# Performance work log

Hardware: AMD Instinct MI355X
Metric: run time of the kernel (lower is better)

The kernel has to match this reference:

```python
import jax, jax.numpy as jnp
import numpy as np

DIM = 4096
N_HEADS_Q = 32
N_HEADS_KV = 8
N_REP = N_HEADS_Q // N_HEADS_KV
HEAD_DIM = DIM // N_HEADS_Q


def setup_inputs() -> dict:
    key = jax.random.key(0)
    k0, k1, k2, k3, k4 = jax.random.split(key, 5)
    B, S = 2, 2048
    scale = 1.0 / np.sqrt(DIM)
    return {
        "x": jax.random.normal(k0, (B, S, DIM), dtype=jnp.float32),
        "wq": jax.random.normal(k1, (DIM, N_HEADS_Q * HEAD_DIM), dtype=jnp.float32) * scale,
        "wk": jax.random.normal(k2, (DIM, N_HEADS_KV * HEAD_DIM), dtype=jnp.float32) * scale,
        "wv": jax.random.normal(k3, (DIM, N_HEADS_KV * HEAD_DIM), dtype=jnp.float32) * scale,
        "wo": jax.random.normal(k4, (DIM, DIM), dtype=jnp.float32) * scale,
        "start_pos": 0,
    }


def reference(x, wq, wk, wv, wo, start_pos):
    # use_cache=False path: fresh causal self-attention with GQA.
    B, S, _ = x.shape
    q = (x @ wq).reshape(B, S, N_HEADS_Q, HEAD_DIM)
    k = (x @ wk).reshape(B, S, N_HEADS_KV, HEAD_DIM)
    v = (x @ wv).reshape(B, S, N_HEADS_KV, HEAD_DIM)
    # repeat_kv: each kv head repeated N_REP times contiguously along head axis
    k = jnp.repeat(k, N_REP, axis=2)  # [B, S, Hq, D]
    v = jnp.repeat(v, N_REP, axis=2)
    att = jnp.einsum("bqhd,bkhd->bhqk", q, k) / np.sqrt(HEAD_DIM).astype(np.float32)
    causal = jnp.tril(jnp.ones((S, S), dtype=bool))  # [S, S]
    att = jnp.where(causal[None, None, :, :], att, -jnp.inf)
    scores = jax.nn.softmax(att, axis=-1)
    out = jnp.einsum("bhqk,bkhd->bqhd", scores, v).reshape(B, S, DIM)
    return out @ wo
```

## Files before the change

### kernel.cpp

```cpp
#include <hip/hip_runtime.h>
#include <cstdint>


typedef __bf16 bf16;
typedef __bf16 bf16x4 __attribute__((ext_vector_type(4)));
typedef __bf16 bf16x8 __attribute__((ext_vector_type(8)));
typedef float f32x4 __attribute__((ext_vector_type(4)));
typedef float f32x16 __attribute__((ext_vector_type(16)));

#define DEV_INLINE __device__ __forceinline__

DEV_INLINE void load_lds16(const bf16* g, bf16* l) {
  __builtin_amdgcn_global_load_lds(
      (const __attribute__((address_space(1))) void*)g,
      (__attribute__((address_space(3))) void*)l, 16, 0, 0);
}

DEV_INLINE unsigned pk2(float a, float b) {
  union { bf16 v[2]; unsigned u; } t;
  t.v[0] = (bf16)a; t.v[1] = (bf16)b;
  return t.u;
}

__global__ __launch_bounds__(256) void cast_f32_bf16(const float* __restrict__ in,
                                                     bf16* __restrict__ out, int n) {
  int i = (blockIdx.x * 256 + threadIdx.x) * 8;
  if (i >= n) return;
  float4 a = *(const float4*)(in + i);
  float4 b = *(const float4*)(in + i + 4);
  bf16x8 o;
  o[0] = (bf16)a.x; o[1] = (bf16)a.y; o[2] = (bf16)a.z; o[3] = (bf16)a.w;
  o[4] = (bf16)b.x; o[5] = (bf16)b.y; o[6] = (bf16)b.z; o[7] = (bf16)b.w;
  *(bf16x8*)(out + i) = o;
}

__global__ __launch_bounds__(256) void transpose_cast_all(
    const float* __restrict__ wq, const float* __restrict__ wk,
    const float* __restrict__ wv, const float* __restrict__ wo,
    bf16* __restrict__ wt, bf16* __restrict__ wot, float qscale) {
  __shared__ float t[32][33];
  int bx = blockIdx.x, k0 = blockIdx.y * 32;
  const float* src;
  bf16* dst;
  int N, ncol0, nrow0;
  float scale = 1.0f;
  if (bx < 128) {
    src = wq; dst = wt; N = 4096; ncol0 = bx * 32; nrow0 = ncol0; scale = qscale;
  } else if (bx < 160) {
    src = wk; dst = wt; N = 1024; ncol0 = (bx - 128) * 32; nrow0 = 4096 + ncol0;
  } else if (bx < 192) {
    src = wv; dst = wt; N = 1024; ncol0 = (bx - 160) * 32; nrow0 = 5120 + ncol0;
  } else {
    src = wo; dst = wot; N = 4096; ncol0 = (bx - 192) * 32; nrow0 = ncol0;
  }
  int tx = threadIdx.x, ty = threadIdx.y;
#pragma unroll
  for (int i = 0; i < 32; i += 8)
    t[ty + i][tx] = src[(size_t)(k0 + ty + i) * N + ncol0 + tx];
  __syncthreads();
#pragma unroll
  for (int i = 0; i < 32; i += 8)
    dst[(size_t)(nrow0 + ty + i) * 4096 + k0 + tx] = (bf16)(t[tx][ty + i] * scale);
}

__global__ __launch_bounds__(256) void transpose_v(const bf16* __restrict__ qkv,
                                                   bf16* __restrict__ vt) {
  __shared__ bf16 t[32][33];
  int s0 = blockIdx.x * 32, d0 = blockIdx.y * 32, bh = blockIdx.z;
  int b = bh >> 3, h = bh & 7;
  int tx = threadIdx.x, ty = threadIdx.y;
#pragma unroll
  for (int i = 0; i < 32; i += 8)
    t[ty + i][tx] =
        qkv[(size_t)(b * 2048 + s0 + ty + i) * 6144 + 5120 + h * 128 + d0 + tx];
  __syncthreads();
#pragma unroll
  for (int i = 0; i < 32; i += 8)
    vt[((size_t)bh * 128 + d0 + ty + i) * 2048 + s0 + tx] = t[tx][ty + i];
}

template <typename OT>
__global__ __launch_bounds__(512, 2) void gemm_bt8(const bf16* __restrict__ A,
                                                   const bf16* __restrict__ Bt,
                                                   OT* __restrict__ C,
                                                   int M, int N, int K) {
  __shared__ __align__(16) bf16 lds[2][4][128 * 64];
  const int t = threadIdx.x, w = t >> 6, l = t & 63;
  const int lr = l & 15, lh = l >> 4;
  const int rm = w >> 2, cn = w & 3;
  const int mBase = blockIdx.y * 256, nBase = blockIdx.x * 256;
  const int NT = K >> 6;

  size_t gA0[2], gB0[2];
#pragma unroll
  for (int it = 0; it < 2; it++) {
    int c = it * 512 + t;
    int idx = c >> 3;
    int kc = (c & 7) ^ (idx & 7);
    gA0[it] = (size_t)(mBase + (idx >> 6) * 128 + (idx & 63)) * K + kc * 8;
    gB0[it] = (size_t)(nBase + (idx >> 5) * 64 + (idx & 31)) * K + kc * 8;
  }
  const size_t strideA1 = (size_t)64 * K;
  const size_t strideB1 = (size_t)32 * K;
  const int ldst0 = (w * 64) * 8, ldst1 = (512 + w * 64) * 8;

#define STAGE_Q(tile, q, base, off0, off1)                                  \
  do {                                                                      \
    int th_ = (tile);                                                       \
    if (th_ < NT) {                                                         \
      bf16* qb_ = &lds[th_ & 1][q][0];                                      \
      size_t ka_ = (size_t)th_ * 64;                                        \
      load_lds16((base) + (off0) + ka_, qb_ + ldst0);                       \
      load_lds16((base) + (off1) + ka_, qb_ + ldst1);                       \
    }                                                                       \
  } while (0)
#define STAGE_A0(tile) STAGE_Q(tile, 0, A, gA0[0], gA0[1])
#define STAGE_B0(tile) STAGE_Q(tile, 1, Bt, gB0[0], gB0[1])
#define STAGE_B1(tile) STAGE_Q(tile, 2, Bt, gB0[0] + strideB1, gB0[1] + strideB1)
#define STAGE_A1(tile) STAGE_Q(tile, 3, A, gA0[0] + strideA1, gA0[1] + strideA1)

  STAGE_A0(0); STAGE_B0(0); STAGE_B1(0); STAGE_A1(0);
  STAGE_A0(1); STAGE_B0(1); STAGE_B1(1);

  f32x4 acc[8][4] = {};
  bf16x8 aF[4][2], bLo[2][2], bHi[2][2];
  const int rowA = (rm * 64 + lr) * 64;
  const int colB = (cn * 32 + lr) * 64;
  const int xo0 = ((lh ^ (lr & 7)) << 3);
  const int xo1 = (((4 + lh) ^ (lr & 7)) << 3);

  for (int T = 0; T < NT; T++) {
    if (T < NT - 1) asm volatile("s_waitcnt vmcnt(6)" ::: "memory");
    else            asm volatile("s_waitcnt vmcnt(0)" ::: "memory");
    __builtin_amdgcn_s_barrier();
    const bf16* q0 = &lds[T & 1][0][0];
    const bf16* q1 = &lds[T & 1][1][0];
    const bf16* q2 = &lds[T & 1][2][0];
    const bf16* q3 = &lds[T & 1][3][0];

#pragma unroll
    for (int mi = 0; mi < 4; mi++) {
      aF[mi][0] = *(const bf16x8*)(q0 + rowA + mi * 1024 + xo0);
      aF[mi][1] = *(const bf16x8*)(q0 + rowA + mi * 1024 + xo1);
    }
#pragma unroll
    for (int ni = 0; ni < 2; ni++) {
      bLo[ni][0] = *(const bf16x8*)(q1 + colB + ni * 1024 + xo0);
      bLo[ni][1] = *(const bf16x8*)(q1 + colB + ni * 1024 + xo1);
    }
    STAGE_A1(T + 1);

    __builtin_amdgcn_s_setprio(1);
#pragma unroll
    for (int ks = 0; ks < 2; ks++)
#pragma unroll
      for (int mi = 0; mi < 4; mi++)
#pragma unroll
        for (int ni = 0; ni < 2; ni++)
          acc[mi][ni] = __builtin_amdgcn_mfma_f32_16x16x32_bf16(
              aF[mi][ks], bLo[ni][ks], acc[mi][ni], 0, 0, 0);
    __builtin_amdgcn_s_setprio(0);
#pragma unroll
    for (int ni = 0; ni < 2; ni++) {
      bHi[ni][0] = *(const bf16x8*)(q2 + colB + ni * 1024 + xo0);
      bHi[ni][1] = *(const bf16x8*)(q2 + colB + ni * 1024 + xo1);
    }

    __builtin_amdgcn_sched_barrier(0);
    __builtin_amdgcn_s_barrier();
    __builtin_amdgcn_sched_barrier(0);
    STAGE_A0(T + 2);

    __builtin_amdgcn_s_setprio(1);
#pragma unroll
    for (int ks = 0; ks < 2; ks++)
#pragma unroll
      for (int mi = 0; mi < 4; mi++)
#pragma unroll
        for (int ni = 0; ni < 2; ni++)
          acc[mi][2 + ni] = __builtin_amdgcn_mfma_f32_16x16x32_bf16(
              aF[mi][ks], bHi[ni][ks], acc[mi][2 + ni], 0, 0, 0);
    __builtin_amdgcn_s_setprio(0);
#pragma unroll
    for (int mi = 0; mi < 4; mi++) {
      aF[mi][0] = *(const bf16x8*)(q3 + rowA + mi * 1024 + xo0);
      aF[mi][1] = *(const bf16x8*)(q3 + rowA + mi * 1024 + xo1);
    }
    STAGE_B0(T + 2);

    __builtin_amdgcn_s_setprio(1);
#pragma unroll
    for (int ks = 0; ks < 2; ks++)
#pragma unroll
      for (int mi = 0; mi < 4; mi++)
#pragma unroll
        for (int ni = 0; ni < 2; ni++)
          acc[4 + mi][ni] = __builtin_amdgcn_mfma_f32_16x16x32_bf16(
              aF[mi][ks], bLo[ni][ks], acc[4 + mi][ni], 0, 0, 0);
    __builtin_amdgcn_s_setprio(0);
    STAGE_B1(T + 2);

    __builtin_amdgcn_s_setprio(1);
#pragma unroll
    for (int ks = 0; ks < 2; ks++)
#pragma unroll
      for (int mi = 0; mi < 4; mi++)
#pragma unroll
        for (int ni = 0; ni < 2; ni++)
          acc[4 + mi][2 + ni] = __builtin_amdgcn_mfma_f32_16x16x32_bf16(
              aF[mi][ks], bHi[ni][ks], acc[4 + mi][2 + ni], 0, 0, 0);
    __builtin_amdgcn_s_setprio(0);
  }
#undef STAGE_Q
#undef STAGE_A0
#undef STAGE_B0
#undef STAGE_B1
#undef STAGE_A1

#pragma unroll
  for (int mi = 0; mi < 8; mi++)
#pragma unroll
    for (int ni = 0; ni < 4; ni++) {
      int row = mBase + rm * 128 + mi * 16 + lh * 4;
      int col = nBase + cn * 64 + ni * 16 + lr;
#pragma unroll
      for (int r = 0; r < 4; r++)
        C[(size_t)(row + r) * N + col] = (OT)acc[mi][ni][r];
    }
}

__global__ __launch_bounds__(256, 2) void flash_attn(const bf16* __restrict__ qkv,
                                                     const bf16* __restrict__ vt,
                                                     bf16* __restrict__ ao) {
  __shared__ __align__(16) bf16 Ks[2][64 * 128];
  __shared__ __align__(16) bf16 Vts[2][128 * 64];
  const int t = threadIdx.x, w = t >> 6, l = t & 63;
  const int l31 = l & 31, hi = l >> 5;
  const int h = blockIdx.y, b = blockIdx.z;
  const int hkv = h >> 2;

#define STAGE_KV(kt_, buf_)                                                   \
  do {                                                                        \
    const int kb_ = (kt_) * 64;                                               \
    _Pragma("unroll")                                                         \
    for (int p = 0; p < 4; p++) {                                             \
      int c = p * 256 + t;                                                    \
      int ldsoff = (p * 256 + w * 64) * 8;                                    \
      int krow = c >> 4, kj = (c & 15) ^ (krow & 15);                         \
      load_lds16(qkv + (size_t)(b * 2048 + kb_ + krow) * 6144 + 4096 +        \
                     hkv * 128 + kj * 8,                                      \
                 &Ks[buf_][ldsoff]);                                          \
      int vrow = c >> 3, vj = (c & 7) ^ (vrow & 7);                           \
      load_lds16(vt + ((size_t)(b * 8 + hkv) * 128 + vrow) * 2048 + kb_ +     \
                     vj * 8,                                                  \
                 &Vts[buf_][ldsoff]);                                         \
    }                                                                         \
  } while (0)

  for (int phase = 0; phase < 2; phase++) {
    const int qt = phase == 0 ? blockIdx.x : 15 - blockIdx.x;
    const int qrow0 = qt * 128 + w * 32;
    const int nkt = 2 * qt + 2;
    const int q = qrow0 + l31;

    STAGE_KV(0, 0);

    bf16x8 qf[8];
#pragma unroll
    for (int d0 = 0; d0 < 8; d0++)
      qf[d0] = *(const bf16x8*)&qkv[(size_t)(b * 2048 + q) * 6144 + h * 128 +
                                    d0 * 16 + hi * 8];

    f32x16 oacc[4] = {};
    float mrow = -3.0e38f, lsum = 0.f;

    asm volatile("s_waitcnt vmcnt(0)" ::: "memory");
    __builtin_amdgcn_s_barrier();

    for (int kt = 0; kt < nkt; kt++) {
      const int cur = kt & 1;
      const int kbase = kt * 64;
      if (kt + 1 < nkt) STAGE_KV(kt + 1, cur ^ 1);

      f32x16 s[2] = {};
      __builtin_amdgcn_s_setprio(1);
#pragma unroll
      for (int d0 = 0; d0 < 8; d0++)
#pragma unroll
        for (int ct = 0; ct < 2; ct++) {
          int krow = ct * 32 + l31;
          bf16x8 kf = *(const bf16x8*)&Ks[cur][(krow * 16 +
                                                ((d0 * 2 + hi) ^ (krow & 15))) * 8];
          s[ct] = __builtin_amdgcn_mfma_f32_32x32x16_bf16(kf, qf[d0], s[ct], 0, 0, 0);
        }
      __builtin_amdgcn_s_setprio(0);

      if (kt >= 2 * qt) {
#pragma unroll
        for (int ct = 0; ct < 2; ct++)
#pragma unroll
          for (int reg = 0; reg < 16; reg++) {
            int ki = kbase + ct * 32 + (reg & 3) + 8 * (reg >> 2) + 4 * hi;
            if (ki > q) s[ct][reg] = -3.0e38f;
          }
      }

      float tm[16];
#pragma unroll
      for (int i = 0; i < 16; i++) tm[i] = fmaxf(s[0][i], s[1][i]);
#pragma unroll
      for (int st = 8; st > 0; st >>= 1)
#pragma unroll
        for (int i = 0; i < 8; i++)
          if (i < st) tm[i] = fmaxf(tm[i], tm[i + st]);
      float mx = fmaxf(tm[0], __shfl_xor(tm[0], 32));
      float mnew = fmaxf(mrow, mx);
      float al = exp2f(mrow - mnew);
      mrow = mnew;
#pragma unroll
      for (int ct = 0; ct < 2; ct++)
#pragma unroll
        for (int reg = 0; reg < 16; reg++) s[ct][reg] = exp2f(s[ct][reg] - mnew);
      float ts[16];
#pragma unroll
      for (int i = 0; i < 16; i++) ts[i] = s[0][i] + s[1][i];
#pragma unroll
      for (int st = 8; st > 0; st >>= 1)
#pragma unroll
        for (int i = 0; i < 8; i++)
          if (i < st) ts[i] = ts[i] + ts[i + st];
      float rs = ts[0] + __shfl_xor(ts[0], 32);
      lsum = lsum * al + rs;

#pragma unroll
      for (int db = 0; db < 4; db++)
#pragma unroll
        for (int reg = 0; reg < 16; reg++) oacc[db][reg] *= al;

      bf16x8 pb[4];
#pragma unroll
      for (int ks = 0; ks < 4; ks++) {
        const int ct = ks >> 1, s1 = ks & 1;
        unsigned A0 = pk2(s[ct][(2 * s1) * 4 + 0], s[ct][(2 * s1) * 4 + 1]);
        unsigned A1 = pk2(s[ct][(2 * s1) * 4 + 2], s[ct][(2 * s1) * 4 + 3]);
        unsigned B0 = pk2(s[ct][(2 * s1 + 1) * 4 + 0], s[ct][(2 * s1 + 1) * 4 + 1]);
        unsigned B1 = pk2(s[ct][(2 * s1 + 1) * 4 + 2], s[ct][(2 * s1 + 1) * 4 + 3]);
        unsigned z0 = hi ? A0 : B0, z1 = hi ? A1 : B1;
        unsigned x0 = __shfl_xor(z0, 32), x1 = __shfl_xor(z1, 32);
        union { unsigned u[4]; bf16x8 v; } pw;
        pw.u[0] = hi ? x0 : A0;
        pw.u[1] = hi ? x1 : A1;
        pw.u[2] = hi ? B0 : x0;
        pw.u[3] = hi ? B1 : x1;
        pb[ks] = pw.v;
      }

      __builtin_amdgcn_s_setprio(1);
#pragma unroll
      for (int ks = 0; ks < 4; ks++)
#pragma unroll
        for (int db = 0; db < 4; db++) {
          int vr = db * 32 + l31;
          bf16x8 vf = *(const bf16x8*)&Vts[cur][(vr * 8 +
                                                 ((ks * 2 + hi) ^ (vr & 7))) * 8];
          oacc[db] = __builtin_amdgcn_mfma_f32_32x32x16_bf16(vf, pb[ks], oacc[db], 0, 0, 0);
        }
      __builtin_amdgcn_s_setprio(0);

      asm volatile("s_waitcnt vmcnt(0)" ::: "memory");
      __builtin_amdgcn_s_barrier();
    }

    float inv = 1.0f / lsum;
#pragma unroll
    for (int db = 0; db < 4; db++)
#pragma unroll
      for (int q4 = 0; q4 < 4; q4++) {
        bf16x4 o4;
#pragma unroll
        for (int j = 0; j < 4; j++) o4[j] = (bf16)(oacc[db][q4 * 4 + j] * inv);
        int d0 = db * 32 + q4 * 8 + hi * 4;
        *(bf16x4*)&ao[(size_t)(b * 2048 + q) * 4096 + h * 128 + d0] = o4;
      }
  }
#undef STAGE_KV
}

extern "C" void kernel_launch(void* const* d_in, const int* in_sizes, int n_in,
                              void* d_out, int out_size, void* d_ws, size_t ws_size,
                              hipStream_t stream) {
  const float* x = (const float*)d_in[0];
  const float* wq = (const float*)d_in[1];
  const float* wk = (const float*)d_in[2];
  const float* wv = (const float*)d_in[3];
  const float* wo = (const float*)d_in[4];
  float* out = (float*)d_out;

  char* ws = (char*)d_ws;
  bf16* xb = (bf16*)(ws + 0);
  bf16* wt = (bf16*)(ws + 33554432);
  bf16* wot = (bf16*)(ws + 83886080);
  bf16* qkv = (bf16*)(ws + 117440512);
  bf16* vt = (bf16*)(ws + 167772160);
  bf16* ao = (bf16*)(ws + 176160768);
  if (ws_size < 209715200u) return;

  const float qscale = 0.08838834764831845f * 1.4426950408889634f;

  cast_f32_bf16<<<8192, 256, 0, stream>>>(x, xb, 16777216);
  transpose_cast_all<<<dim3(320, 128), dim3(32, 8), 0, stream>>>(
      wq, wk, wv, wo, wt, wot, qscale);

  gemm_bt8<bf16><<<dim3(24, 16), 512, 0, stream>>>(xb, wt, qkv, 4096, 6144, 4096);
  transpose_v<<<dim3(64, 4, 16), dim3(32, 8), 0, stream>>>(qkv, vt);
  flash_attn<<<dim3(8, 32, 2), 256, 0, stream>>>(qkv, vt, ao);
  gemm_bt8<float><<<dim3(16, 16), 512, 0, stream>>>(ao, wot, out, 4096, 4096, 4096);
}
```

Measured before the change: 667.7 us.

## Retile QKV GEMM to 256x192 blocks and widen weight transpose tiles

The GEMM is templated on the number of 64-column B units, with LDS reorganised into 64x64 units. The QKV projection now uses 256x192 tiles, giving 512 blocks instead of 384 so the work balances better across the CUs. The weight transpose-cast kernel moves to 64x64 tiles with float4 loads and bf16x4 stores to cut memory transactions. The narrower tile lowers arithmetic intensity per block, and the vmcnt wait counts are hand-tuned to each variant, which risks subtle pipeline mistakes.

```diff
diff --git a/kernel.cpp b/kernel.cpp
--- a/kernel.cpp
+++ b/kernel.cpp
@@ -38,29 +38,39 @@
     const float* __restrict__ wq, const float* __restrict__ wk,
     const float* __restrict__ wv, const float* __restrict__ wo,
     bf16* __restrict__ wt, bf16* __restrict__ wot, float qscale) {
-  __shared__ float t[32][33];
-  int bx = blockIdx.x, k0 = blockIdx.y * 32;
+  __shared__ float sm[64][65];
+  const int bx = blockIdx.x, k0 = blockIdx.y * 64;
   const float* src;
   bf16* dst;
   int N, ncol0, nrow0;
   float scale = 1.0f;
-  if (bx < 128) {
-    src = wq; dst = wt; N = 4096; ncol0 = bx * 32; nrow0 = ncol0; scale = qscale;
-  } else if (bx < 160) {
-    src = wk; dst = wt; N = 1024; ncol0 = (bx - 128) * 32; nrow0 = 4096 + ncol0;
-  } else if (bx < 192) {
-    src = wv; dst = wt; N = 1024; ncol0 = (bx - 160) * 32; nrow0 = 5120 + ncol0;
+  if (bx < 64) {
+    src = wq; dst = wt; N = 4096; ncol0 = bx * 64; nrow0 = ncol0; scale = qscale;
+  } else if (bx < 80) {
+    src = wk; dst = wt; N = 1024; ncol0 = (bx - 64) * 64; nrow0 = 4096 + ncol0;
+  } else if (bx < 96) {
+    src = wv; dst = wt; N = 1024; ncol0 = (bx - 80) * 64; nrow0 = 5120 + ncol0;
   } else {
-    src = wo; dst = wot; N = 4096; ncol0 = (bx - 192) * 32; nrow0 = ncol0;
-  }
-  int tx = threadIdx.x, ty = threadIdx.y;
-#pragma unroll
-  for (int i = 0; i < 32; i += 8)
-    t[ty + i][tx] = src[(size_t)(k0 + ty + i) * N + ncol0 + tx];
+    src = wo; dst = wot; N = 4096; ncol0 = (bx - 96) * 64; nrow0 = ncol0;
+  }
+  const int t = threadIdx.x;
+  const int r16 = t >> 4, c4 = (t & 15) * 4;
+#pragma unroll
+  for (int i = 0; i < 4; i++) {
+    int row = r16 + i * 16;
+    float4 v = *(const float4*)&src[(size_t)(k0 + row) * N + ncol0 + c4];
+    sm[row][c4 + 0] = v.x; sm[row][c4 + 1] = v.y;
+    sm[row][c4 + 2] = v.z; sm[row][c4 + 3] = v.w;
+  }
   __syncthreads();
 #pragma unroll
-  for (int i = 0; i < 32; i += 8)
-    dst[(size_t)(nrow0 + ty + i) * 4096 + k0 + tx] = (bf16)(t[tx][ty + i] * scale);
+  for (int i = 0; i < 4; i++) {
+    int nr = r16 + i * 16;
+    bf16x4 o;
+#pragma unroll
+    for (int j = 0; j < 4; j++) o[j] = (bf16)(sm[c4 + j][nr] * scale);
+    *(bf16x4*)&dst[(size_t)(nrow0 + nr) * 4096 + k0 + c4] = o;
+  }
 }
 
 __global__ __launch_bounds__(256) void transpose_v(const bf16* __restrict__ qkv,
@@ -79,76 +89,80 @@
     vt[((size_t)bh * 128 + d0 + ty + i) * 2048 + s0 + tx] = t[tx][ty + i];
 }
 
-template <typename OT>
+template <typename OT, int NBU>
 __global__ __launch_bounds__(512, 2) void gemm_bt8(const bf16* __restrict__ A,
                                                    const bf16* __restrict__ Bt,
                                                    OT* __restrict__ C,
                                                    int M, int N, int K) {
-  __shared__ __align__(16) bf16 lds[2][4][128 * 64];
+  constexpr int NU = 4 + NBU;
+  __shared__ __align__(16) bf16 lds[2][NU][64 * 64];
   const int t = threadIdx.x, w = t >> 6, l = t & 63;
   const int lr = l & 15, lh = l >> 4;
   const int rm = w >> 2, cn = w & 3;
-  const int mBase = blockIdx.y * 256, nBase = blockIdx.x * 256;
+  const int mBase = blockIdx.y * 256, nBase = blockIdx.x * (NBU * 64);
   const int NT = K >> 6;
 
-  size_t gA0[2], gB0[2];
-#pragma unroll
-  for (int it = 0; it < 2; it++) {
-    int c = it * 512 + t;
-    int idx = c >> 3;
-    int kc = (c & 7) ^ (idx & 7);
-    gA0[it] = (size_t)(mBase + (idx >> 6) * 128 + (idx & 63)) * K + kc * 8;
-    gB0[it] = (size_t)(nBase + (idx >> 5) * 64 + (idx & 31)) * K + kc * 8;
-  }
-  const size_t strideA1 = (size_t)64 * K;
-  const size_t strideB1 = (size_t)32 * K;
-  const int ldst0 = (w * 64) * 8, ldst1 = (512 + w * 64) * 8;
-
-#define STAGE_Q(tile, q, base, off0, off1)                                  \
-  do {                                                                      \
-    int th_ = (tile);                                                       \
-    if (th_ < NT) {                                                         \
-      bf16* qb_ = &lds[th_ & 1][q][0];                                      \
-      size_t ka_ = (size_t)th_ * 64;                                        \
-      load_lds16((base) + (off0) + ka_, qb_ + ldst0);                       \
-      load_lds16((base) + (off1) + ka_, qb_ + ldst1);                       \
-    }                                                                       \
+  const int idx = t >> 3;
+  const int kc = (t & 7) ^ (idx & 7);
+  const size_t u64K = (size_t)64 * K;
+  const size_t gA = (size_t)(mBase + idx) * K + kc * 8;
+  const size_t gB = (size_t)(nBase + idx) * K + kc * 8;
+
+#define STAGE_U(tile_, u_)                                                   \
+  do {                                                                       \
+    int th_ = (tile_);                                                       \
+    if (th_ < NT) {                                                          \
+      const bf16* src_ = ((u_) < 4 ? A + gA + (size_t)(u_)*u64K              \
+                                   : Bt + gB + (size_t)((u_)-4) * u64K) +    \
+                         (size_t)th_ * 64;                                   \
+      load_lds16(src_, &lds[th_ & 1][u_][w * 512]);                          \
+    }                                                                        \
   } while (0)
-#define STAGE_A0(tile) STAGE_Q(tile, 0, A, gA0[0], gA0[1])
-#define STAGE_B0(tile) STAGE_Q(tile, 1, Bt, gB0[0], gB0[1])
-#define STAGE_B1(tile) STAGE_Q(tile, 2, Bt, gB0[0] + strideB1, gB0[1] + strideB1)
-#define STAGE_A1(tile) STAGE_Q(tile, 3, A, gA0[0] + strideA1, gA0[1] + strideA1)
-
-  STAGE_A0(0); STAGE_B0(0); STAGE_B1(0); STAGE_A1(0);
-  STAGE_A0(1); STAGE_B0(1); STAGE_B1(1);
-
-  f32x4 acc[8][4] = {};
-  bf16x8 aF[4][2], bLo[2][2], bHi[2][2];
-  const int rowA = (rm * 64 + lr) * 64;
-  const int colB = (cn * 32 + lr) * 64;
+
+  STAGE_U(0, 0); STAGE_U(0, 2);
+#pragma unroll
+  for (int u = 4; u < NU; u++) STAGE_U(0, u);
+  STAGE_U(0, 1); STAGE_U(0, 3);
+  STAGE_U(1, 0); STAGE_U(1, 2);
+#pragma unroll
+  for (int u = 4; u < NU; u++) STAGE_U(1, u);
+
+  constexpr int NLO = 2, NHI = NBU - 2;
+  f32x4 acc[8][NBU] = {};
+  bf16x8 aF[4][2], bLo[NLO][2], bHi[NHI][2];
   const int xo0 = ((lh ^ (lr & 7)) << 3);
   const int xo1 = (((4 + lh) ^ (lr & 7)) << 3);
+  int uB[NBU], oB[NBU];
+#pragma unroll
+  for (int ni = 0; ni < NBU; ni++) {
+    int colb = cn * (NBU * 16) + ni * 16;
+    uB[ni] = 4 + (colb >> 6);
+    oB[ni] = ((colb & 63) + lr) * 64;
+  }
 
   for (int T = 0; T < NT; T++) {
-    if (T < NT - 1) asm volatile("s_waitcnt vmcnt(6)" ::: "memory");
-    else            asm volatile("s_waitcnt vmcnt(0)" ::: "memory");
+    if (T < NT - 1) {
+      if constexpr (NBU == 3) asm volatile("s_waitcnt vmcnt(5)" ::: "memory");
+      else                    asm volatile("s_waitcnt vmcnt(6)" ::: "memory");
+    } else {
+      asm volatile("s_waitcnt vmcnt(0)" ::: "memory");
+    }
     __builtin_amdgcn_s_barrier();
-    const bf16* q0 = &lds[T & 1][0][0];
-    const bf16* q1 = &lds[T & 1][1][0];
-    const bf16* q2 = &lds[T & 1][2][0];
-    const bf16* q3 = &lds[T & 1][3][0];
+    const int par = T & 1;
 
 #pragma unroll
     for (int mi = 0; mi < 4; mi++) {
-      aF[mi][0] = *(const bf16x8*)(q0 + rowA + mi * 1024 + xo0);
-      aF[mi][1] = *(const bf16x8*)(q0 + rowA + mi * 1024 + xo1);
-    }
-#pragma unroll
-    for (int ni = 0; ni < 2; ni++) {
-      bLo[ni][0] = *(const bf16x8*)(q1 + colB + ni * 1024 + xo0);
-      bLo[ni][1] = *(const bf16x8*)(q1 + colB + ni * 1024 + xo1);
-    }
-    STAGE_A1(T + 1);
+      const bf16* qa = &lds[par][rm * 2][(mi * 16 + lr) * 64];
+      aF[mi][0] = *(const bf16x8*)(qa + xo0);
+      aF[mi][1] = *(const bf16x8*)(qa + xo1);
+    }
+#pragma unroll
+    for (int ni = 0; ni < NLO; ni++) {
+      const bf16* qb = &lds[par][uB[ni]][oB[ni]];
+      bLo[ni][0] = *(const bf16x8*)(qb + xo0);
+      bLo[ni][1] = *(const bf16x8*)(qb + xo1);
+    }
+    STAGE_U(T + 1, 1); STAGE_U(T + 1, 3);
 
     __builtin_amdgcn_s_setprio(1);
 #pragma unroll
@@ -156,20 +170,21 @@
 #pragma unroll
       for (int mi = 0; mi < 4; mi++)
 #pragma unroll
-        for (int ni = 0; ni < 2; ni++)
+        for (int ni = 0; ni < NLO; ni++)
           acc[mi][ni] = __builtin_amdgcn_mfma_f32_16x16x32_bf16(
               aF[mi][ks], bLo[ni][ks], acc[mi][ni], 0, 0, 0);
     __builtin_amdgcn_s_setprio(0);
 #pragma unroll
-    for (int ni = 0; ni < 2; ni++) {
-      bHi[ni][0] = *(const bf16x8*)(q2 + colB + ni * 1024 + xo0);
-      bHi[ni][1] = *(const bf16x8*)(q2 + colB + ni * 1024 + xo1);
+    for (int ni = 0; ni < NHI; ni++) {
+      const bf16* qb = &lds[par][uB[NLO + ni]][oB[NLO + ni]];
+      bHi[ni][0] = *(const bf16x8*)(qb + xo0);
+      bHi[ni][1] = *(const bf16x8*)(qb + xo1);
     }
 
     __builtin_amdgcn_sched_barrier(0);
     __builtin_amdgcn_s_barrier();
     __builtin_amdgcn_sched_barrier(0);
-    STAGE_A0(T + 2);
+    STAGE_U(T + 2, 0); STAGE_U(T + 2, 2);
 
     __builtin_amdgcn_s_setprio(1);
 #pragma unroll
@@ -177,16 +192,17 @@
 #pragma unroll
       for (int mi = 0; mi < 4; mi++)
 #pragma unroll
-        for (int ni = 0; ni < 2; ni++)
-          acc[mi][2 + ni] = __builtin_amdgcn_mfma_f32_16x16x32_bf16(
-              aF[mi][ks], bHi[ni][ks], acc[mi][2 + ni], 0, 0, 0);
+        for (int ni = 0; ni < NHI; ni++)
+          acc[mi][NLO + ni] = __builtin_amdgcn_mfma_f32_16x16x32_bf16(
+              aF[mi][ks], bHi[ni][ks], acc[mi][NLO + ni], 0, 0, 0);
     __builtin_amdgcn_s_setprio(0);
 #pragma unroll
     for (int mi = 0; mi < 4; mi++) {
-      aF[mi][0] = *(const bf16x8*)(q3 + rowA + mi * 1024 + xo0);
-      aF[mi][1] = *(const bf16x8*)(q3 + rowA + mi * 1024 + xo1);
-    }
-    STAGE_B0(T + 2);
+      const bf16* qa = &lds[par][rm * 2 + 1][(mi * 16 + lr) * 64];
+      aF[mi][0] = *(const bf16x8*)(qa + xo0);
+      aF[mi][1] = *(const bf16x8*)(qa + xo1);
+    }
+    STAGE_U(T + 2, 4); STAGE_U(T + 2, 5);
 
     __builtin_amdgcn_s_setprio(1);
 #pragma unroll
@@ -194,11 +210,12 @@
 #pragma unroll
       for (int mi = 0; mi < 4; mi++)
 #pragma unroll
-        for (int ni = 0; ni < 2; ni++)
+        for (int ni = 0; ni < NLO; ni++)
           acc[4 + mi][ni] = __builtin_amdgcn_mfma_f32_16x16x32_bf16(
               aF[mi][ks], bLo[ni][ks], acc[4 + mi][ni], 0, 0, 0);
     __builtin_amdgcn_s_setprio(0);
-    STAGE_B1(T + 2);
+#pragma unroll
+    for (int u = 6; u < NU; u++) STAGE_U(T + 2, u);
 
     __builtin_amdgcn_s_setprio(1);
 #pragma unroll
@@ -206,23 +223,19 @@
 #pragma unroll
       for (int mi = 0; mi < 4; mi++)
 #pragma unroll
-        for (int ni = 0; ni < 2; ni++)
-          acc[4 + mi][2 + ni] = __builtin_amdgcn_mfma_f32_16x16x32_bf16(
-              aF[mi][ks], bHi[ni][ks], acc[4 + mi][2 + ni], 0, 0, 0);
+        for (int ni = 0; ni < NHI; ni++)
+          acc[4 + mi][NLO + ni] = __builtin_amdgcn_mfma_f32_16x16x32_bf16(
+              aF[mi][ks], bHi[ni][ks], acc[4 + mi][NLO + ni], 0, 0, 0);
     __builtin_amdgcn_s_setprio(0);
   }
-#undef STAGE_Q
-#undef STAGE_A0
-#undef STAGE_B0
-#undef STAGE_B1
-#undef STAGE_A1
+#undef STAGE_U
 
 #pragma unroll
   for (int mi = 0; mi < 8; mi++)
 #pragma unroll
-    for (int ni = 0; ni < 4; ni++) {
+    for (int ni = 0; ni < NBU; ni++) {
       int row = mBase + rm * 128 + mi * 16 + lh * 4;
-      int col = nBase + cn * 64 + ni * 16 + lr;
+      int col = nBase + cn * (NBU * 16) + ni * 16 + lr;
 #pragma unroll
       for (int r = 0; r < 4; r++)
         C[(size_t)(row + r) * N + col] = (OT)acc[mi][ni][r];
@@ -408,11 +421,11 @@
   const float qscale = 0.08838834764831845f * 1.4426950408889634f;
 
   cast_f32_bf16<<<8192, 256, 0, stream>>>(x, xb, 16777216);
-  transpose_cast_all<<<dim3(320, 128), dim3(32, 8), 0, stream>>>(
+  transpose_cast_all<<<dim3(160, 64), 256, 0, stream>>>(
       wq, wk, wv, wo, wt, wot, qscale);
 
-  gemm_bt8<bf16><<<dim3(24, 16), 512, 0, stream>>>(xb, wt, qkv, 4096, 6144, 4096);
+  gemm_bt8<bf16, 3><<<dim3(32, 16), 512, 0, stream>>>(xb, wt, qkv, 4096, 6144, 4096);
   transpose_v<<<dim3(64, 4, 16), dim3(32, 8), 0, stream>>>(qkv, vt);
   flash_attn<<<dim3(8, 32, 2), 256, 0, stream>>>(qkv, vt, ao);
-  gemm_bt8<float><<<dim3(16, 16), 512, 0, stream>>>(ao, wot, out, 4096, 4096, 4096);
-}
+  gemm_bt8<float, 4><<<dim3(16, 16), 512, 0, stream>>>(ao, wot, out, 4096, 4096, 4096);
+}
```

After: 650.1 us. 2.6% less time.
